# Performance work log

Measured on AMD Instinct MI355X. Metric: run time of the kernel, lower is better.

The kernel has to match this reference:

```python
import jax, jax.numpy as jnp
import numpy as np
from functools import partial

NUM_GROUP = 512   # S
GROUP_SIZE = 32   # K
BN_EPS = 1e-5
STD_EPS = 1e-5


def fps(xyz, n_samples):
    # xyz: [N,3] -> indices [n_samples] (farthest point sampling, start at idx 0)
    N = xyz.shape[0]
    def body(carry, _):
        dists, last = carry
        d = jnp.sum((xyz - xyz[last]) ** 2, axis=-1)
        dists = jnp.minimum(dists, d)
        nxt = jnp.argmax(dists).astype(jnp.int32)
        return (dists, nxt), last
    init = (jnp.full((N,), jnp.inf, xyz.dtype), jnp.array(0, jnp.int32))
    _, idx = jax.lax.scan(body, init, None, length=n_samples)
    return idx


def knn_idx(xyz, center, k):
    # xyz [N,3], center [S,3] -> k nearest neighbor indices [S,k]
    d2 = (jnp.sum(center ** 2, -1)[:, None] + jnp.sum(xyz ** 2, -1)[None, :]
          - 2.0 * center @ xyz.T)
    _, idx = jax.lax.top_k(-d2, k)
    return idx


def conv1(x, W, b):
    # 1x1 Conv1d: x [M,Cin,L], W [Cout,Cin] -> [M,Cout,L]
    return jnp.einsum('oc,mcl->mol', W, x) + b[None, :, None]


def bn(x, g, b):
    # BatchNorm1d eval mode with running_mean=0, running_var=1
    scale = g / jnp.sqrt(1.0 + BN_EPS)
    return x * scale[None, :, None] + b[None, :, None]


def res_block(x, W1, b1, g1, bb1, W2, b2, g2, bb2):
    # ConvBNReLURes1D, res_expansion=1.0
    h = jax.nn.relu(bn(conv1(x, W1, b1), g1, bb1))
    h = bn(conv1(h, W2, b2), g2, bb2)
    return jax.nn.relu(h + x)


def reference(xyz, alpha, beta, Wt, bt, gt, bbt,
              Wpre1, bpre1, gpre1, bbpre1, Wpre2, bpre2, gpre2, bbpre2,
              Wpos1, bpos1, gpos1, bbpos1, Wpos2, bpos2, gpos2, bbpos2):
    B, N, _ = xyz.shape
    S, K = NUM_GROUP, GROUP_SIZE
    C = Wt.shape[0]

    # ---- LocalGrouper: FPS + KNN + gather + normalize ----
    c_idx = jax.vmap(partial(fps, n_samples=S))(xyz)          # [B,S]
    center = jax.vmap(lambda p, i: p[i])(xyz, c_idx)          # [B,S,3]
    n_idx = jax.vmap(partial(knn_idx, k=K))(xyz, center)      # [B,S,K]
    nbr = jax.vmap(lambda p, i: p[i])(xyz, n_idx)             # [B,S,K,3]

    mean = center[:, :, None, :]
    diff = nbr - mean
    std = jnp.std(diff.reshape(B, -1), axis=-1, ddof=1).reshape(B, 1, 1, 1)
    nbr = alpha * (diff / (std + STD_EPS)) + beta
    grouped = jnp.concatenate(
        [nbr, jnp.broadcast_to(mean, (B, S, K, 3))], axis=-1)  # [B,S,K,6]

    # ---- Extraction ----
    x = grouped.transpose(0, 1, 3, 2).reshape(B * S, 6, K)     # [B*S,6,K]
    h = jax.nn.relu(bn(conv1(x, Wt, bt), gt, bbt))             # [B*S,C,K]
    h = res_block(h, Wpre1, bpre1, gpre1, bbpre1, Wpre2, bpre2, gpre2, bbpre2)
    pooled = jnp.max(h, axis=-1)                               # [B*S,C]
    feat = pooled.reshape(B, S, C).transpose(0, 2, 1)          # [B,C,S]
    feat = res_block(feat, Wpos1, bpos1, gpos1, bbpos1, Wpos2, bpos2, gpos2, bbpos2)
    return feat.transpose(0, 2, 1)                             # [B,S,C]


def setup_inputs() -> dict:
    key = jax.random.key(0)
    ks = jax.random.split(key, 12)
    B, N, C = 8, 8192, 384
    s6 = 1.0 / np.sqrt(6.0)
    sc = 1.0 / np.sqrt(C)
    return {
        'xyz': jax.random.normal(ks[0], (B, N, 3), jnp.float32),
        'alpha': jnp.ones((1, 1, 1, 3), jnp.float32),
        'beta': jnp.zeros((1, 1, 1, 3), jnp.float32),
        'Wt': jax.random.normal(ks[1], (C, 6), jnp.float32) * s6,
        'bt': jax.random.normal(ks[2], (C,), jnp.float32) * 0.02,
        'gt': jnp.ones((C,), jnp.float32), 'bbt': jnp.zeros((C,), jnp.float32),
        'Wpre1': jax.random.normal(ks[3], (C, C), jnp.float32) * sc,
        'bpre1': jax.random.normal(ks[4], (C,), jnp.float32) * 0.02,
        'gpre1': jnp.ones((C,), jnp.float32), 'bbpre1': jnp.zeros((C,), jnp.float32),
        'Wpre2': jax.random.normal(ks[5], (C, C), jnp.float32) * sc,
        'bpre2': jax.random.normal(ks[6], (C,), jnp.float32) * 0.02,
        'gpre2': jnp.ones((C,), jnp.float32), 'bbpre2': jnp.zeros((C,), jnp.float32),
        'Wpos1': jax.random.normal(ks[7], (C, C), jnp.float32) * sc,
        'bpos1': jax.random.normal(ks[8], (C,), jnp.float32) * 0.02,
        'gpos1': jnp.ones((C,), jnp.float32), 'bbpos1': jnp.zeros((C,), jnp.float32),
        'Wpos2': jax.random.normal(ks[9], (C, C), jnp.float32) * sc,
        'bpos2': jax.random.normal(ks[10], (C,), jnp.float32) * 0.02,
        'gpos2': jnp.ones((C,), jnp.float32), 'bbpos2': jnp.zeros((C,), jnp.float32),
    }
```

## Files before the change

### kernel.cpp

```cpp
#include <hip/hip_runtime.h>
#include <hip/hip_bf16.h>
#include <math.h>

typedef __bf16 bf16x8 __attribute__((ext_vector_type(8)));
typedef float f32x4 __attribute__((ext_vector_type(4)));
typedef float f32x2 __attribute__((ext_vector_type(2)));

#define NPTS 8192
#define SGRP 512
#define KNBR 32
#define CCH 384
#define LDSP 392

static __device__ __forceinline__ unsigned short f2b(float f) {
  union { float f; unsigned u; } v; v.f = f;
  return (unsigned short)((v.u + 0x7fffu + ((v.u >> 16) & 1u)) >> 16);
}
static __device__ __forceinline__ float b2f(unsigned short u) {
  union { unsigned u; float f; } v; v.u = ((unsigned)u) << 16;
  return v.f;
}
static __device__ __forceinline__ unsigned pk2(float a, float b) {
  return (unsigned)f2b(a) | ((unsigned)f2b(b) << 16);
}

#define DPPMAX(v, ctrl) \
  fmaxf((v), __int_as_float(__builtin_amdgcn_update_dpp(0, __float_as_int(v), (ctrl), 0xf, 0xf, false)))
#define DPPMIN(v, ctrl) \
  fminf((v), __int_as_float(__builtin_amdgcn_update_dpp(0x7f800000, __float_as_int(v), (ctrl), 0xf, 0xf, false)))

struct FoldArgs {
  const float *W, *b, *g, *bb;
  unsigned short* Wd;
  float* bd;
};
__global__ void fold4_bf16(FoldArgs a0, FoldArgs a1, FoldArgs a2, FoldArgs a3) {
  FoldArgs a = (blockIdx.y == 0) ? a0 : (blockIdx.y == 1) ? a1 : (blockIdx.y == 2) ? a2 : a3;
  int o = blockIdx.x;
  float sc = a.g[o] / sqrtf(1.0f + 1e-5f);
  for (int c = threadIdx.x; c < CCH; c += blockDim.x)
    a.Wd[o * CCH + c] = f2b(a.W[o * CCH + c] * sc);
  if (threadIdx.x == 0) a.bd[o] = a.b[o] * sc + a.bb[o];
}
__global__ void fold_w_f32(const float* __restrict__ W, const float* __restrict__ b,
                           const float* __restrict__ g, const float* __restrict__ bb,
                           float* __restrict__ Wd, float* __restrict__ bd, int Cin) {
  int o = blockIdx.x;
  float sc = g[o] / sqrtf(1.0f + 1e-5f);
  for (int c = threadIdx.x; c < Cin; c += blockDim.x)
    Wd[o * Cin + c] = W[o * Cin + c] * sc;
  if (threadIdx.x == 0) bd[o] = b[o] * sc + bb[o];
}

__global__ __launch_bounds__(1024)
void fps_kernel(const float* __restrict__ xyz, int* __restrict__ cIdx) {
  #pragma clang fp contract(off)
  __shared__ float xs[NPTS], ys[NPTS], zs[NPTS];
  __shared__ float slotV[2][16];
  __shared__ unsigned slotI[2][16];
  const int tid = threadIdx.x, lane = tid & 63, wid = tid >> 6;
  const int b = blockIdx.x;
  const float* xb = xyz + (size_t)b * NPTS * 3;

  f32x2 X2[4], Y2[4], Z2[4], D2[4];
  {
    const float4* s = (const float4*)xb + tid * 6;
    float4 t0 = s[0], t1 = s[1], t2 = s[2], t3 = s[3], t4 = s[4], t5 = s[5];
    X2[0] = (f32x2){t0.x, t0.w}; Y2[0] = (f32x2){t0.y, t1.x}; Z2[0] = (f32x2){t0.z, t1.y};
    X2[1] = (f32x2){t1.z, t2.y}; Y2[1] = (f32x2){t1.w, t2.z}; Z2[1] = (f32x2){t2.x, t2.w};
    X2[2] = (f32x2){t3.x, t3.w}; Y2[2] = (f32x2){t3.y, t4.x}; Z2[2] = (f32x2){t3.z, t4.y};
    X2[3] = (f32x2){t4.z, t5.y}; Y2[3] = (f32x2){t4.w, t5.z}; Z2[3] = (f32x2){t5.x, t5.w};
  }
  #pragma unroll
  for (int j = 0; j < 4; ++j) {
    int p = tid * 8 + j * 2;
    xs[p] = X2[j].x; ys[p] = Y2[j].x; zs[p] = Z2[j].x;
    xs[p + 1] = X2[j].y; ys[p + 1] = Y2[j].y; zs[p + 1] = Z2[j].y;
    D2[j] = (f32x2){__builtin_inff(), __builtin_inff()};
  }
  if (tid == 0) cIdx[b * SGRP] = 0;
  __syncthreads();
  float cx = xs[0], cy = ys[0], cz = zs[0];
  const int tbase = tid * 8;

  for (int step = 1; step < SGRP; ++step) {
    const int par = step & 1;
    const f32x2 cxv = (f32x2){cx, cx}, cyv = (f32x2){cy, cy}, czv = (f32x2){cz, cz};
    float bv = -1.0f; int bi = 0;
    #pragma unroll
    for (int j = 0; j < 4; ++j) {
      f32x2 dx = X2[j] - cxv, dy = Y2[j] - cyv, dz = Z2[j] - czv;
      f32x2 d = (dx * dx + dy * dy) + dz * dz;
      f32x2 nd = __builtin_elementwise_min(D2[j], d);
      D2[j] = nd;
      if (nd.x > bv) { bv = nd.x; bi = tbase + 2 * j; }
      if (nd.y > bv) { bv = nd.y; bi = tbase + 2 * j + 1; }
    }
    float m = bv;
    m = DPPMAX(m, 0x111); m = DPPMAX(m, 0x112); m = DPPMAX(m, 0x114);
    m = DPPMAX(m, 0x118); m = DPPMAX(m, 0x142); m = DPPMAX(m, 0x143);
    float wmax = __uint_as_float(__builtin_amdgcn_readlane(__float_as_uint(m), 63));
    unsigned long long msk = __ballot(bv == wmax);
    int srcLane = (int)__builtin_ctzll(msk);
    unsigned wbi = (unsigned)__builtin_amdgcn_readlane(bi, srcLane);
    if (lane == 0) { slotV[par][wid] = wmax; slotI[par][wid] = wbi; }
    __syncthreads();
    float sv = slotV[par][lane & 15];
    unsigned si = slotI[par][lane & 15];
    float g = sv;
    g = DPPMAX(g, 0x111); g = DPPMAX(g, 0x112); g = DPPMAX(g, 0x114);
    g = DPPMAX(g, 0x118);
    float gm = __uint_as_float(__builtin_amdgcn_readlane(__float_as_uint(g), 15));
    int l0 = (int)__builtin_ctzll(__ballot(sv == gm));
    unsigned gi = (unsigned)__builtin_amdgcn_readlane((int)si, l0);
    if (tid == 0) cIdx[b * SGRP + step] = (int)gi;
    cx = xs[gi]; cy = ys[gi]; cz = zs[gi];
  }
}

__global__ __launch_bounds__(256) void knn_kernel(const float* __restrict__ xyz,
                                                  const int* __restrict__ cIdx,
                                                  float* __restrict__ nbrDiff,
                                                  float* __restrict__ ctrW,
                                                  float* __restrict__ partials) {
  #pragma clang fp contract(off)
  __shared__ unsigned long long keyBuf[4];
  __shared__ int winners[KNBR];
  const int cid = blockIdx.x;
  const int b = cid >> 9;
  const int tid = threadIdx.x;
  const int lane = tid & 63;
  const float* xb = xyz + (size_t)b * NPTS * 3;
  const int cI = cIdx[cid];
  const float cx = xb[cI * 3], cy = xb[cI * 3 + 1], cz = xb[cI * 3 + 2];
  const float cs = (cx * cx + cy * cy) + cz * cz;

  float d2[32];
  float mv = __builtin_inff(); int mi = 0;
  #pragma unroll
  for (int j = 0; j < 32; ++j) {
    int p = tid + (j << 8);
    float x = xb[p * 3], y = xb[p * 3 + 1], z = xb[p * 3 + 2];
    float ps = (x * x + y * y) + z * z;
    float dot = (cx * x + cy * y) + cz * z;
    d2[j] = (cs + ps) - 2.0f * dot;
    if (d2[j] < mv) { mv = d2[j]; mi = p; }
  }
  if (tid < 4) keyBuf[tid] = 0xFFFFFFFFFFFFFFFFull;
  __syncthreads();

  for (int it = 0; it < KNBR; ++it) {
    if (tid == 0) keyBuf[(it + 2) & 3] = 0xFFFFFFFFFFFFFFFFull;
    float m = mv;
    m = DPPMIN(m, 0x111); m = DPPMIN(m, 0x112); m = DPPMIN(m, 0x114);
    m = DPPMIN(m, 0x118); m = DPPMIN(m, 0x142); m = DPPMIN(m, 0x143);
    float wmin = __uint_as_float(__builtin_amdgcn_readlane(__float_as_uint(m), 63));
    unsigned long long msk = __ballot(mv == wmin);
    int src = (int)__builtin_ctzll(msk);
    int wbi = __builtin_amdgcn_readlane(mi, src);
    if (__builtin_popcountll(msk) > 1) {
      unsigned long long rest = msk & (msk - 1);
      while (rest) {
        int l = (int)__builtin_ctzll(rest);
        int cand = __builtin_amdgcn_readlane(mi, l);
        if (cand < wbi) wbi = cand;
        rest &= rest - 1;
      }
    }
    if (lane == 0) {
      unsigned u = __float_as_uint(wmin);
      unsigned mm = u ^ (unsigned)(((int)u >> 31) | 0x80000000);
      unsigned long long key = (((unsigned long long)mm) << 32) | (unsigned long long)(unsigned)wbi;
      atomicMin(&keyBuf[it & 3], key);
    }
    __syncthreads();
    unsigned long long k = keyBuf[it & 3];
    int wi = (int)(k & 0x1FFFu);
    if (tid == 0) winners[it] = wi;
    if (tid == (wi & 255)) {
      #pragma unroll
      for (int j = 0; j < 32; ++j)
        if (wi == tid + (j << 8)) d2[j] = __builtin_inff();
      mv = __builtin_inff(); mi = 0;
      #pragma unroll
      for (int j = 0; j < 32; ++j)
        if (d2[j] < mv) { mv = d2[j]; mi = tid + (j << 8); }
    }
  }
  __syncthreads();

  float sum = 0.f, sq = 0.f;
  if (tid < KNBR) {
    int w = winners[tid];
    float dx = xb[w * 3] - cx, dy = xb[w * 3 + 1] - cy, dz = xb[w * 3 + 2] - cz;
    size_t o = ((size_t)cid * KNBR + tid) * 3;
    nbrDiff[o + 0] = dx; nbrDiff[o + 1] = dy; nbrDiff[o + 2] = dz;
    sum = (dx + dy) + dz;
    sq = (dx * dx + dy * dy) + dz * dz;
  }
  if (tid < 64) {
    #pragma unroll
    for (int s = 1; s < 64; s <<= 1) { sum += __shfl_xor(sum, s); sq += __shfl_xor(sq, s); }
    if (tid == 0) { partials[cid * 2] = sum; partials[cid * 2 + 1] = sq; }
  }
  if (tid < 3) ctrW[(size_t)cid * 3 + tid] = xb[cI * 3 + tid];
}

__global__ __launch_bounds__(256) void std_kernel(const float* __restrict__ partials,
                                                  float* __restrict__ stdv) {
  __shared__ double sd[256], sq[256];
  const int b = blockIdx.x, t = threadIdx.x;
  int i0 = (b * 512 + t) * 2;
  sd[t] = (double)partials[i0] + (double)partials[i0 + 512];
  sq[t] = (double)partials[i0 + 1] + (double)partials[i0 + 513];
  for (int st = 128; st > 0; st >>= 1) {
    __syncthreads();
    if (t < st) { sd[t] += sd[t + st]; sq[t] += sq[t + st]; }
  }
  if (t == 0) {
    double n = (double)(SGRP * KNBR * 3);
    double mean = sd[0] / n;
    double var = (sq[0] - sd[0] * mean) / (n - 1.0);
    stdv[b] = (float)sqrt(var);
  }
}

static __device__ __forceinline__ void gemm_half(const unsigned short* __restrict__ W,
                                                 const unsigned short* ht,
                                                 int oBase, int n0, int r16, int g4,
                                                 f32x4 acc[3][4]) {
  for (int ks = 0; ks < 12; ++ks) {
    const int kOff = ks * 32 + g4 * 8;
    bf16x8 a[3], bb[4];
    #pragma unroll
    for (int i = 0; i < 3; ++i)
      a[i] = *(const bf16x8*)(W + (size_t)(oBase + i * 16 + r16) * CCH + kOff);
    #pragma unroll
    for (int j = 0; j < 4; ++j)
      bb[j] = *(const bf16x8*)(ht + (n0 + j * 16 + r16) * LDSP + kOff);
    #pragma unroll
    for (int i = 0; i < 3; ++i) {
      #pragma unroll
      for (int j = 0; j < 4; ++j)
        acc[i][j] = __builtin_amdgcn_mfma_f32_16x16x32_bf16(a[i], bb[j], acc[i][j], 0, 0, 0);
    }
  }
}

__global__ __launch_bounds__(512) void group_mlp_kernel(
    const float* __restrict__ alpha, const float* __restrict__ beta,
    const float* __restrict__ WtF, const float* __restrict__ btF,
    const unsigned short* __restrict__ W1, const float* __restrict__ b1,
    const unsigned short* __restrict__ W2, const float* __restrict__ b2,
    const float* __restrict__ nbrDiff, const float* __restrict__ ctrW,
    const float* __restrict__ stdv, unsigned short* __restrict__ feat) {
  __shared__ unsigned short ht[128 * LDSP];
  __shared__ float xtw[128 * 8];
  __shared__ float wtl[CCH * 6];
  __shared__ float btl[CCH];

  const int tid = threadIdx.x;
  const int lane = tid & 63, wid = tid >> 6;
  const int r16 = lane & 15, g4 = lane >> 4;
  const int bid = blockIdx.x;
  const int b = bid >> 7;
  const int sBase = (bid & 127) << 2;

  for (int i = tid; i < CCH * 6; i += 512) wtl[i] = WtF[i];
  for (int i = tid; i < CCH; i += 512) btl[i] = btF[i];

  const float inv = 1.0f / (stdv[b] + 1e-5f);
  if (tid < 128) {
    int g = tid >> 5, kk = tid & 31;
    int cid = b * SGRP + sBase + g;
    const float* nb = nbrDiff + ((size_t)cid * KNBR + kk) * 3;
    const float* cc = ctrW + (size_t)cid * 3;
    #pragma unroll
    for (int c = 0; c < 3; ++c) {
      xtw[tid * 8 + c] = alpha[c] * (nb[c] * inv) + beta[c];
      xtw[tid * 8 + 3 + c] = cc[c];
    }
  }
  __syncthreads();

  {
    int l = tid & 127, oi = tid >> 7;
    float xv[6];
    #pragma unroll
    for (int c = 0; c < 6; ++c) xv[c] = xtw[l * 8 + c];
    for (int j = 0; j < 96; ++j) {
      int o = oi * 96 + j;
      float v = btl[o];
      #pragma unroll
      for (int c = 0; c < 6; ++c) v += wtl[o * 6 + c] * xv[c];
      ht[l * LDSP + o] = f2b(fmaxf(v, 0.0f));
    }
  }
  __syncthreads();

  const int oBase = wid * 48;

  for (int half = 0; half < 2; ++half) {
    const int n0 = half * 64;
    f32x4 acc[3][4];
    #pragma unroll
    for (int i = 0; i < 3; ++i) {
      #pragma unroll
      for (int j = 0; j < 4; ++j) acc[i][j] = (f32x4){0.f, 0.f, 0.f, 0.f};
    }
    gemm_half(W1, ht, oBase, n0, r16, g4, acc);
    __syncthreads();
    #pragma unroll
    for (int i = 0; i < 3; ++i) {
      int o4 = oBase + i * 16 + g4 * 4;
      float bs0 = b1[o4], bs1 = b1[o4 + 1], bs2 = b1[o4 + 2], bs3 = b1[o4 + 3];
      #pragma unroll
      for (int j = 0; j < 4; ++j) {
        int row = n0 + j * 16 + r16;
        unsigned u0 = pk2(fmaxf(acc[i][j][0] + bs0, 0.f), fmaxf(acc[i][j][1] + bs1, 0.f));
        unsigned u1 = pk2(fmaxf(acc[i][j][2] + bs2, 0.f), fmaxf(acc[i][j][3] + bs3, 0.f));
        *(uint2*)(ht + row * LDSP + o4) = make_uint2(u0, u1);
      }
    }
    __syncthreads();
  }

  for (int half = 0; half < 2; ++half) {
    const int n0 = half * 64;
    f32x4 acc[3][4];
    #pragma unroll
    for (int i = 0; i < 3; ++i) {
      #pragma unroll
      for (int j = 0; j < 4; ++j) acc[i][j] = (f32x4){0.f, 0.f, 0.f, 0.f};
    }
    gemm_half(W2, ht, oBase, n0, r16, g4, acc);

    float bias2[3][4];
    #pragma unroll
    for (int i = 0; i < 3; ++i) {
      int o4 = oBase + i * 16 + g4 * 4;
      #pragma unroll
      for (int r = 0; r < 4; ++r) bias2[i][r] = b2[o4 + r];
    }
    float mx[3][2][4];
    #pragma unroll
    for (int i = 0; i < 3; ++i) {
      #pragma unroll
      for (int gg = 0; gg < 2; ++gg) {
        #pragma unroll
        for (int r = 0; r < 4; ++r) mx[i][gg][r] = 0.f;
      }
    }
    #pragma unroll
    for (int j = 0; j < 4; ++j) {
      int l = n0 + j * 16 + r16;
      float xv[6];
      #pragma unroll
      for (int c = 0; c < 6; ++c) xv[c] = xtw[l * 8 + c];
      #pragma unroll
      for (int i = 0; i < 3; ++i) {
        int o4 = oBase + i * 16 + g4 * 4;
        #pragma unroll
        for (int r = 0; r < 4; ++r) {
          float h0 = btl[o4 + r];
          #pragma unroll
          for (int c = 0; c < 6; ++c) h0 += wtl[(o4 + r) * 6 + c] * xv[c];
          h0 = fmaxf(h0, 0.f);
          float v = fmaxf(acc[i][j][r] + bias2[i][r] + h0, 0.f);
          mx[i][j >> 1][r] = fmaxf(mx[i][j >> 1][r], v);
        }
      }
    }
    #pragma unroll
    for (int i = 0; i < 3; ++i) {
      #pragma unroll
      for (int gg = 0; gg < 2; ++gg) {
        float m0 = mx[i][gg][0], m1 = mx[i][gg][1], m2 = mx[i][gg][2], m3 = mx[i][gg][3];
        #pragma unroll
        for (int s = 1; s < 16; s <<= 1) {
          m0 = fmaxf(m0, __shfl_xor(m0, s));
          m1 = fmaxf(m1, __shfl_xor(m1, s));
          m2 = fmaxf(m2, __shfl_xor(m2, s));
          m3 = fmaxf(m3, __shfl_xor(m3, s));
        }
        if (r16 == 0) {
          int sIdx = sBase + half * 2 + gg;
          size_t fi = ((size_t)(b * SGRP + sIdx)) * CCH + oBase + i * 16 + g4 * 4;
          *(uint2*)(feat + fi) = make_uint2(pk2(m0, m1), pk2(m2, m3));
        }
      }
    }
  }
}

__global__ __launch_bounds__(256) void pos_kernel(const unsigned short* __restrict__ feat,
                                                  const unsigned short* __restrict__ Wp1,
                                                  const float* __restrict__ bp1,
                                                  const unsigned short* __restrict__ Wp2,
                                                  const float* __restrict__ bp2,
                                                  float* __restrict__ out) {
  __shared__ unsigned short h1[16 * LDSP];
  const int tid = threadIdx.x;
  const int lane = tid & 63, wid = tid >> 6;
  const int r16 = lane & 15, g4 = lane >> 4;
  const int bid = blockIdx.x;
  const int b = bid >> 5;
  const int s0 = (bid & 31) << 4;
  const size_t rowBase = ((size_t)(b * SGRP + s0 + r16)) * CCH;

  f32x4 acc[6];
  #pragma unroll
  for (int i = 0; i < 6; ++i) acc[i] = (f32x4){0.f, 0.f, 0.f, 0.f};
  for (int ks = 0; ks < 12; ++ks) {
    const int kOff = ks * 32 + g4 * 8;
    bf16x8 bfr = *(const bf16x8*)(feat + rowBase + kOff);
    #pragma unroll
    for (int i = 0; i < 6; ++i) {
      bf16x8 a = *(const bf16x8*)(Wp1 + (size_t)(wid * 96 + i * 16 + r16) * CCH + kOff);
      acc[i] = __builtin_amdgcn_mfma_f32_16x16x32_bf16(a, bfr, acc[i], 0, 0, 0);
    }
  }
  #pragma unroll
  for (int i = 0; i < 6; ++i) {
    int o4 = wid * 96 + i * 16 + g4 * 4;
    unsigned u0 = pk2(fmaxf(acc[i][0] + bp1[o4 + 0], 0.f), fmaxf(acc[i][1] + bp1[o4 + 1], 0.f));
    unsigned u1 = pk2(fmaxf(acc[i][2] + bp1[o4 + 2], 0.f), fmaxf(acc[i][3] + bp1[o4 + 3], 0.f));
    *(uint2*)(h1 + r16 * LDSP + o4) = make_uint2(u0, u1);
  }
  __syncthreads();

  f32x4 acc2[6];
  #pragma unroll
  for (int i = 0; i < 6; ++i) acc2[i] = (f32x4){0.f, 0.f, 0.f, 0.f};
  for (int ks = 0; ks < 12; ++ks) {
    const int kOff = ks * 32 + g4 * 8;
    bf16x8 bfr = *(const bf16x8*)(h1 + r16 * LDSP + kOff);
    #pragma unroll
    for (int i = 0; i < 6; ++i) {
      bf16x8 a = *(const bf16x8*)(Wp2 + (size_t)(wid * 96 + i * 16 + r16) * CCH + kOff);
      acc2[i] = __builtin_amdgcn_mfma_f32_16x16x32_bf16(a, bfr, acc2[i], 0, 0, 0);
    }
  }
  #pragma unroll
  for (int i = 0; i < 6; ++i) {
    int o4 = wid * 96 + i * 16 + g4 * 4;
    uint2 rr = *(const uint2*)(feat + rowBase + o4);
    float4 v;
    v.x = fmaxf(acc2[i][0] + bp2[o4 + 0] + b2f((unsigned short)(rr.x & 0xffff)), 0.f);
    v.y = fmaxf(acc2[i][1] + bp2[o4 + 1] + b2f((unsigned short)(rr.x >> 16)), 0.f);
    v.z = fmaxf(acc2[i][2] + bp2[o4 + 2] + b2f((unsigned short)(rr.y & 0xffff)), 0.f);
    v.w = fmaxf(acc2[i][3] + bp2[o4 + 3] + b2f((unsigned short)(rr.y >> 16)), 0.f);
    *(float4*)(out + rowBase + o4) = v;
  }
}

extern "C" void kernel_launch(void* const* d_in, const int* in_sizes, int n_in,
                              void* d_out, int out_size, void* d_ws, size_t ws_size,
                              hipStream_t stream) {
  (void)in_sizes; (void)n_in; (void)out_size; (void)ws_size;
  const float* xyz   = (const float*)d_in[0];
  const float* alpha = (const float*)d_in[1];
  const float* beta  = (const float*)d_in[2];
  const float* Wt    = (const float*)d_in[3];
  const float* bt    = (const float*)d_in[4];
  const float* gt    = (const float*)d_in[5];
  const float* bbt   = (const float*)d_in[6];
  const float* Wpre1 = (const float*)d_in[7];
  const float* bpre1 = (const float*)d_in[8];
  const float* gpre1 = (const float*)d_in[9];
  const float* bbpre1= (const float*)d_in[10];
  const float* Wpre2 = (const float*)d_in[11];
  const float* bpre2 = (const float*)d_in[12];
  const float* gpre2 = (const float*)d_in[13];
  const float* bbpre2= (const float*)d_in[14];
  const float* Wpos1 = (const float*)d_in[15];
  const float* bpos1 = (const float*)d_in[16];
  const float* gpos1 = (const float*)d_in[17];
  const float* bbpos1= (const float*)d_in[18];
  const float* Wpos2 = (const float*)d_in[19];
  const float* bpos2 = (const float*)d_in[20];
  const float* gpos2 = (const float*)d_in[21];
  const float* bbpos2= (const float*)d_in[22];

  char* ws = (char*)d_ws;
  size_t off = 0;
  auto alloc = [&](size_t bytes) -> void* {
    void* p = ws + off;
    off += (bytes + 255) & ~(size_t)255;
    return p;
  };
  float* WtF = (float*)alloc(CCH * 6 * 4);
  float* btF = (float*)alloc(CCH * 4);
  unsigned short* W1 = (unsigned short*)alloc(CCH * CCH * 2);
  float* b1 = (float*)alloc(CCH * 4);
  unsigned short* W2 = (unsigned short*)alloc(CCH * CCH * 2);
  float* b2 = (float*)alloc(CCH * 4);
  unsigned short* Wp1 = (unsigned short*)alloc(CCH * CCH * 2);
  float* bp1 = (float*)alloc(CCH * 4);
  unsigned short* Wp2 = (unsigned short*)alloc(CCH * CCH * 2);
  float* bp2 = (float*)alloc(CCH * 4);
  int* cIdx = (int*)alloc(8 * SGRP * 4);
  float* ctrW = (float*)alloc(8 * SGRP * 3 * 4);
  float* nbrD = (float*)alloc((size_t)8 * SGRP * KNBR * 3 * 4);
  float* partials = (float*)alloc(8 * SGRP * 2 * 4);
  float* stdv = (float*)alloc(8 * 4);
  unsigned short* feat = (unsigned short*)alloc((size_t)8 * SGRP * CCH * 2);

  fold_w_f32<<<CCH, 64, 0, stream>>>(Wt, bt, gt, bbt, WtF, btF, 6);
  FoldArgs fa0{Wpre1, bpre1, gpre1, bbpre1, W1, b1};
  FoldArgs fa1{Wpre2, bpre2, gpre2, bbpre2, W2, b2};
  FoldArgs fa2{Wpos1, bpos1, gpos1, bbpos1, Wp1, bp1};
  FoldArgs fa3{Wpos2, bpos2, gpos2, bbpos2, Wp2, bp2};
  fold4_bf16<<<dim3(CCH, 4), 128, 0, stream>>>(fa0, fa1, fa2, fa3);

  fps_kernel<<<8, 1024, 0, stream>>>(xyz, cIdx);
  knn_kernel<<<8 * SGRP, 256, 0, stream>>>(xyz, cIdx, nbrD, ctrW, partials);
  std_kernel<<<8, 256, 0, stream>>>(partials, stdv);
  group_mlp_kernel<<<1024, 512, 0, stream>>>(alpha, beta, WtF, btF, W1, b1, W2, b2,
                                             nbrD, ctrW, stdv, feat);
  pos_kernel<<<256, 256, 0, stream>>>(feat, Wp1, bp1, Wp2, bp2, (float*)d_out);
}
```

Before: 1.0000 ms.

## Process two batches per FPS block to share one barrier per step

Each FPS workgroup now handles two point clouds at once, keeping both in registers and doing both argmax reductions before a single __syncthreads per step. The second batch's centroid coordinates are fetched from global memory instead of LDS. The aim is to interleave two independent latency-bound dependency chains, roughly halving the number of barrier-separated serial steps across the grid. In exchange it doubles register pressure, runs only 4 blocks (using fewer CUs), and adds a global-memory load on the critical path of every step.

```diff
diff --git a/kernel.cpp b/kernel.cpp
--- a/kernel.cpp
+++ b/kernel.cpp
@@ -56,65 +56,114 @@
 void fps_kernel(const float* __restrict__ xyz, int* __restrict__ cIdx) {
   #pragma clang fp contract(off)
   __shared__ float xs[NPTS], ys[NPTS], zs[NPTS];
-  __shared__ float slotV[2][16];
-  __shared__ unsigned slotI[2][16];
+  __shared__ float slotV[2][2][16];
+  __shared__ unsigned slotI[2][2][16];
   const int tid = threadIdx.x, lane = tid & 63, wid = tid >> 6;
-  const int b = blockIdx.x;
-  const float* xb = xyz + (size_t)b * NPTS * 3;
-
-  f32x2 X2[4], Y2[4], Z2[4], D2[4];
+  const int b0 = blockIdx.x * 2, b1 = b0 + 1;
+  const float* xA = xyz + (size_t)b0 * NPTS * 3;
+  const float* xB = xyz + (size_t)b1 * NPTS * 3;
+
+  f32x2 XA[4], YA[4], ZA[4], DA[4];
+  f32x2 XB[4], YB[4], ZB[4], DB[4];
   {
-    const float4* s = (const float4*)xb + tid * 6;
+    const float4* s = (const float4*)xA + tid * 6;
     float4 t0 = s[0], t1 = s[1], t2 = s[2], t3 = s[3], t4 = s[4], t5 = s[5];
-    X2[0] = (f32x2){t0.x, t0.w}; Y2[0] = (f32x2){t0.y, t1.x}; Z2[0] = (f32x2){t0.z, t1.y};
-    X2[1] = (f32x2){t1.z, t2.y}; Y2[1] = (f32x2){t1.w, t2.z}; Z2[1] = (f32x2){t2.x, t2.w};
-    X2[2] = (f32x2){t3.x, t3.w}; Y2[2] = (f32x2){t3.y, t4.x}; Z2[2] = (f32x2){t3.z, t4.y};
-    X2[3] = (f32x2){t4.z, t5.y}; Y2[3] = (f32x2){t4.w, t5.z}; Z2[3] = (f32x2){t5.x, t5.w};
+    XA[0] = (f32x2){t0.x, t0.w}; YA[0] = (f32x2){t0.y, t1.x}; ZA[0] = (f32x2){t0.z, t1.y};
+    XA[1] = (f32x2){t1.z, t2.y}; YA[1] = (f32x2){t1.w, t2.z}; ZA[1] = (f32x2){t2.x, t2.w};
+    XA[2] = (f32x2){t3.x, t3.w}; YA[2] = (f32x2){t3.y, t4.x}; ZA[2] = (f32x2){t3.z, t4.y};
+    XA[3] = (f32x2){t4.z, t5.y}; YA[3] = (f32x2){t4.w, t5.z}; ZA[3] = (f32x2){t5.x, t5.w};
+  }
+  {
+    const float4* s = (const float4*)xB + tid * 6;
+    float4 t0 = s[0], t1 = s[1], t2 = s[2], t3 = s[3], t4 = s[4], t5 = s[5];
+    XB[0] = (f32x2){t0.x, t0.w}; YB[0] = (f32x2){t0.y, t1.x}; ZB[0] = (f32x2){t0.z, t1.y};
+    XB[1] = (f32x2){t1.z, t2.y}; YB[1] = (f32x2){t1.w, t2.z}; ZB[1] = (f32x2){t2.x, t2.w};
+    XB[2] = (f32x2){t3.x, t3.w}; YB[2] = (f32x2){t3.y, t4.x}; ZB[2] = (f32x2){t3.z, t4.y};
+    XB[3] = (f32x2){t4.z, t5.y}; YB[3] = (f32x2){t4.w, t5.z}; ZB[3] = (f32x2){t5.x, t5.w};
   }
   #pragma unroll
   for (int j = 0; j < 4; ++j) {
     int p = tid * 8 + j * 2;
-    xs[p] = X2[j].x; ys[p] = Y2[j].x; zs[p] = Z2[j].x;
-    xs[p + 1] = X2[j].y; ys[p + 1] = Y2[j].y; zs[p + 1] = Z2[j].y;
-    D2[j] = (f32x2){__builtin_inff(), __builtin_inff()};
-  }
-  if (tid == 0) cIdx[b * SGRP] = 0;
+    xs[p] = XA[j].x; ys[p] = YA[j].x; zs[p] = ZA[j].x;
+    xs[p + 1] = XA[j].y; ys[p + 1] = YA[j].y; zs[p + 1] = ZA[j].y;
+    DA[j] = (f32x2){__builtin_inff(), __builtin_inff()};
+    DB[j] = (f32x2){__builtin_inff(), __builtin_inff()};
+  }
+  if (tid == 0) { cIdx[b0 * SGRP] = 0; cIdx[b1 * SGRP] = 0; }
   __syncthreads();
-  float cx = xs[0], cy = ys[0], cz = zs[0];
+  float cxA = xA[0], cyA = xA[1], czA = xA[2];
+  float cxB = xB[0], cyB = xB[1], czB = xB[2];
   const int tbase = tid * 8;
 
   for (int step = 1; step < SGRP; ++step) {
     const int par = step & 1;
-    const f32x2 cxv = (f32x2){cx, cx}, cyv = (f32x2){cy, cy}, czv = (f32x2){cz, cz};
-    float bv = -1.0f; int bi = 0;
-    #pragma unroll
-    for (int j = 0; j < 4; ++j) {
-      f32x2 dx = X2[j] - cxv, dy = Y2[j] - cyv, dz = Z2[j] - czv;
-      f32x2 d = (dx * dx + dy * dy) + dz * dz;
-      f32x2 nd = __builtin_elementwise_min(D2[j], d);
-      D2[j] = nd;
-      if (nd.x > bv) { bv = nd.x; bi = tbase + 2 * j; }
-      if (nd.y > bv) { bv = nd.y; bi = tbase + 2 * j + 1; }
-    }
-    float m = bv;
-    m = DPPMAX(m, 0x111); m = DPPMAX(m, 0x112); m = DPPMAX(m, 0x114);
-    m = DPPMAX(m, 0x118); m = DPPMAX(m, 0x142); m = DPPMAX(m, 0x143);
-    float wmax = __uint_as_float(__builtin_amdgcn_readlane(__float_as_uint(m), 63));
-    unsigned long long msk = __ballot(bv == wmax);
-    int srcLane = (int)__builtin_ctzll(msk);
-    unsigned wbi = (unsigned)__builtin_amdgcn_readlane(bi, srcLane);
-    if (lane == 0) { slotV[par][wid] = wmax; slotI[par][wid] = wbi; }
+    {
+      const f32x2 cxv = (f32x2){cxA, cxA}, cyv = (f32x2){cyA, cyA}, czv = (f32x2){czA, czA};
+      float bv = -1.0f; int bi = 0;
+      #pragma unroll
+      for (int j = 0; j < 4; ++j) {
+        f32x2 dx = XA[j] - cxv, dy = YA[j] - cyv, dz = ZA[j] - czv;
+        f32x2 d = (dx * dx + dy * dy) + dz * dz;
+        f32x2 nd = __builtin_elementwise_min(DA[j], d);
+        DA[j] = nd;
+        if (nd.x > bv) { bv = nd.x; bi = tbase + 2 * j; }
+        if (nd.y > bv) { bv = nd.y; bi = tbase + 2 * j + 1; }
+      }
+      float m = bv;
+      m = DPPMAX(m, 0x111); m = DPPMAX(m, 0x112); m = DPPMAX(m, 0x114);
+      m = DPPMAX(m, 0x118); m = DPPMAX(m, 0x142); m = DPPMAX(m, 0x143);
+      float wmax = __uint_as_float(__builtin_amdgcn_readlane(__float_as_uint(m), 63));
+      unsigned long long msk = __ballot(bv == wmax);
+      int srcLane = (int)__builtin_ctzll(msk);
+      unsigned wbi = (unsigned)__builtin_amdgcn_readlane(bi, srcLane);
+      if (lane == 0) { slotV[par][0][wid] = wmax; slotI[par][0][wid] = wbi; }
+    }
+    {
+      const f32x2 cxv = (f32x2){cxB, cxB}, cyv = (f32x2){cyB, cyB}, czv = (f32x2){czB, czB};
+      float bv = -1.0f; int bi = 0;
+      #pragma unroll
+      for (int j = 0; j < 4; ++j) {
+        f32x2 dx = XB[j] - cxv, dy = YB[j] - cyv, dz = ZB[j] - czv;
+        f32x2 d = (dx * dx + dy * dy) + dz * dz;
+        f32x2 nd = __builtin_elementwise_min(DB[j], d);
+        DB[j] = nd;
+        if (nd.x > bv) { bv = nd.x; bi = tbase + 2 * j; }
+        if (nd.y > bv) { bv = nd.y; bi = tbase + 2 * j + 1; }
+      }
+      float m = bv;
+      m = DPPMAX(m, 0x111); m = DPPMAX(m, 0x112); m = DPPMAX(m, 0x114);
+      m = DPPMAX(m, 0x118); m = DPPMAX(m, 0x142); m = DPPMAX(m, 0x143);
+      float wmax = __uint_as_float(__builtin_amdgcn_readlane(__float_as_uint(m), 63));
+      unsigned long long msk = __ballot(bv == wmax);
+      int srcLane = (int)__builtin_ctzll(msk);
+      unsigned wbi = (unsigned)__builtin_amdgcn_readlane(bi, srcLane);
+      if (lane == 0) { slotV[par][1][wid] = wmax; slotI[par][1][wid] = wbi; }
+    }
     __syncthreads();
-    float sv = slotV[par][lane & 15];
-    unsigned si = slotI[par][lane & 15];
-    float g = sv;
-    g = DPPMAX(g, 0x111); g = DPPMAX(g, 0x112); g = DPPMAX(g, 0x114);
-    g = DPPMAX(g, 0x118);
-    float gm = __uint_as_float(__builtin_amdgcn_readlane(__float_as_uint(g), 15));
-    int l0 = (int)__builtin_ctzll(__ballot(sv == gm));
-    unsigned gi = (unsigned)__builtin_amdgcn_readlane((int)si, l0);
-    if (tid == 0) cIdx[b * SGRP + step] = (int)gi;
-    cx = xs[gi]; cy = ys[gi]; cz = zs[gi];
+    {
+      float sv = slotV[par][0][lane & 15];
+      unsigned si = slotI[par][0][lane & 15];
+      float g = sv;
+      g = DPPMAX(g, 0x111); g = DPPMAX(g, 0x112); g = DPPMAX(g, 0x114);
+      g = DPPMAX(g, 0x118);
+      float gm = __uint_as_float(__builtin_amdgcn_readlane(__float_as_uint(g), 15));
+      int l0 = (int)__builtin_ctzll(__ballot(sv == gm));
+      unsigned gi = (unsigned)__builtin_amdgcn_readlane((int)si, l0);
+      if (tid == 0) cIdx[b0 * SGRP + step] = (int)gi;
+      cxA = xs[gi]; cyA = ys[gi]; czA = zs[gi];
+    }
+    {
+      float sv = slotV[par][1][lane & 15];
+      unsigned si = slotI[par][1][lane & 15];
+      float g = sv;
+      g = DPPMAX(g, 0x111); g = DPPMAX(g, 0x112); g = DPPMAX(g, 0x114);
+      g = DPPMAX(g, 0x118);
+      float gm = __uint_as_float(__builtin_amdgcn_readlane(__float_as_uint(g), 15));
+      int l0 = (int)__builtin_ctzll(__ballot(sv == gm));
+      unsigned gi = (unsigned)__builtin_amdgcn_readlane((int)si, l0);
+      if (tid == 0) cIdx[b1 * SGRP + step] = (int)gi;
+      cxB = xB[gi * 3 + 0]; cyB = xB[gi * 3 + 1]; czB = xB[gi * 3 + 2];
+    }
   }
 }
 
@@ -513,7 +562,7 @@
   FoldArgs fa3{Wpos2, bpos2, gpos2, bbpos2, Wp2, bp2};
   fold4_bf16<<<dim3(CCH, 4), 128, 0, stream>>>(fa0, fa1, fa2, fa3);
 
-  fps_kernel<<<8, 1024, 0, stream>>>(xyz, cIdx);
+  fps_kernel<<<4, 1024, 0, stream>>>(xyz, cIdx);
   knn_kernel<<<8 * SGRP, 256, 0, stream>>>(xyz, cIdx, nbrD, ctrW, partials);
   std_kernel<<<8, 256, 0, stream>>>(partials, stdv);
   group_mlp_kernel<<<1024, 512, 0, stream>>>(alpha, beta, WtF, btF, W1, b1, W2, b2,
```

Measured after the change: 1.475 ms. +47.5%, slower.
